# Optimization experiments

Hardware: AMD Instinct MI355X
Metric: run time of the kernel (lower is better)

Reference implementation:

```python
import jax, jax.numpy as jnp
import numpy as np

SAME_RANGE = 1.0  # forward() default same_range
FLOW_SCALE = 32.0  # realistic pixel displacements


def setup_inputs() -> dict:
    key = jax.random.key(0)
    k1, k2, k3 = jax.random.split(key, 3)
    H, W, C = 2160, 3840, 3
    img = jax.random.uniform(k1, (H, W, C), dtype=jnp.float32)
    flow = jax.random.normal(k2, (H, W, 2), dtype=jnp.float32) * FLOW_SCALE
    depth = jax.random.uniform(k3, (H, W), dtype=jnp.float32) * 100.0 + 0.1
    return {"img": img, "flow": flow, "depth": depth}


def reference(img, flow, depth):
    """Forward warping with depth z-buffer occlusion resolution.

    Each source pixel (y,x) is scattered to p1 = p0 + flow (clamped to the
    image). At each target cell, only the contributions whose depth is within
    SAME_RANGE of the minimum arriving depth survive; surviving contributions
    are averaged. Empty cells stay zero (matches np.zeros_like init in the
    original C-library warp).
    """
    H, W, C = img.shape
    N = H * W
    gy, gx = jnp.meshgrid(jnp.arange(H, dtype=flow.dtype),
                          jnp.arange(W, dtype=flow.dtype), indexing='ij')
    # safe_x / safe_y clamped target coordinates
    tx = jnp.clip(gx + flow[..., 0], 0.0, W - 1)
    ty = jnp.clip(gy + flow[..., 1], 0.0, H - 1)
    ix = jnp.round(tx).astype(jnp.int32)
    iy = jnp.round(ty).astype(jnp.int32)
    idx = jax.lax.stop_gradient((iy * W + ix).reshape(N))  # [N] flat targets

    d = depth.reshape(N)
    # z-buffer: min depth landing at each target cell
    zmin = jnp.full((N,), jnp.inf, dtype=d.dtype).at[idx].min(d)
    keep = (d <= zmin[idx] + SAME_RANGE).astype(img.dtype)  # [N]

    src = img.reshape(N, C) * keep[:, None]
    num = jnp.zeros((N, C), dtype=img.dtype).at[idx].add(src)
    cnt = jnp.zeros((N,), dtype=img.dtype).at[idx].add(keep)
    out = jnp.where(cnt[:, None] > 0, num / jnp.maximum(cnt, 1.0)[:, None], 0.0)
    return out.reshape(H, W, C)
```

## Files before the change

### kernel.cpp

```cpp
#include <hip/hip_runtime.h>

#define HH 2160
#define WW 3840
#define NN (HH * WW)

#define SROWS 2
#define NSTRIP (HH / SROWS)
#define CPS (SROWS * WW)

#define BTH 256
#define GRP 2
#define GPX 4
#define RPT (GRP * GPX)
#define PXB (BTH * RPT)

#define ICAP 12288
#define ECAP 262144
#define E0BASE ((u32)NSTRIP * ICAP)
#define E1BASE (E0BASE + ECAP)
#define TOTAL_RECS ((size_t)E1BASE + ECAP)

typedef unsigned long long u64;
typedef unsigned int u32;

__device__ __forceinline__ u32 strip_base(int s) {
    if (s == 0) return E0BASE;
    if (s == NSTRIP - 1) return E1BASE;
    return (u32)s * ICAP;
}


__global__ __launch_bounds__(256) void init_cursor_kernel(u32* __restrict__ cursor)
{
    int s = blockIdx.x * blockDim.x + threadIdx.x;
    if (s < NSTRIP) cursor[s] = strip_base(s);
}

__global__ __launch_bounds__(BTH, 6) void scatter_kernel(
    const float4* __restrict__ img4,
    const float4* __restrict__ flow4,
    const float4* __restrict__ depth4,
    u32* __restrict__ cursor,
    u64* __restrict__ recs)
{
    __shared__ u32 lc[1088];
    __shared__ u32 gb[1088];

    const int t = threadIdx.x;
    for (int s = t; s < 1088; s += BTH) lc[s] = 0;
    __syncthreads();

    const int wb = blockIdx.x * PXB;
    const int p0 = wb + t * GPX;
    const int p1 = wb + BTH * GPX + t * GPX;

    float4 fa0 = flow4[(p0 >> 1) + 0], fb0 = flow4[(p0 >> 1) + 1];
    float4 fa1 = flow4[(p1 >> 1) + 0], fb1 = flow4[(p1 >> 1) + 1];
    float4 dv0 = depth4[p0 >> 2];
    float4 dv1 = depth4[p1 >> 2];
    int ib0 = (p0 * 3) >> 2, ib1 = (p1 * 3) >> 2;
    float4 a0 = img4[ib0 + 0], a1 = img4[ib0 + 1], a2 = img4[ib0 + 2];
    float4 c0 = img4[ib1 + 0], c1 = img4[ib1 + 1], c2 = img4[ib1 + 2];

    u64 rrec[GRP][GPX];
    u32 aux[GRP][GPX];

    #pragma unroll
    for (int g = 0; g < GRP; ++g) {
        int p = g ? p1 : p0;
        int y = p / WW;
        int x = p - y * WW;
        float4 fa = g ? fa1 : fa0, fb = g ? fb1 : fb0;
        float4 dv = g ? dv1 : dv0;
        float4 i0 = g ? c0 : a0, i1 = g ? c1 : a1, i2 = g ? c2 : a2;
        float fx[GPX] = { fa.x, fa.z, fb.x, fb.z };
        float fy[GPX] = { fa.y, fa.w, fb.y, fb.w };
        float rr[GPX] = { i0.x, i0.w, i1.z, i2.y };
        float gg[GPX] = { i0.y, i1.x, i1.w, i2.z };
        float bb[GPX] = { i0.z, i1.y, i2.x, i2.w };
        float dd[GPX] = { dv.x, dv.y, dv.z, dv.w };
        #pragma unroll
        for (int k = 0; k < GPX; ++k) {
            float tx = fminf(fmaxf((float)(x + k) + fx[k], 0.0f), (float)(WW - 1));
            float ty = fminf(fmaxf((float)y + fy[k], 0.0f), (float)(HH - 1));
            int ix = (int)rintf(tx);
            int iy = (int)rintf(ty);
            int st = iy >> 1;
            u32 cell = (u32)((iy & 1) * WW + ix);
            u32 rq = (u32)(rr[k] * 63.0f + 0.5f);
            u32 gq = (u32)(gg[k] * 127.0f + 0.5f);
            u32 bq = (u32)(bb[k] * 63.0f + 0.5f);
            rrec[g][k] = ((u64)__float_as_uint(dd[k]) << 32)
                       | ((u64)cell << 19)
                       | (u64)(rq | (gq << 6) | (bq << 13));
            u32 rank = atomicAdd(&lc[st], 1u);
            aux[g][k] = ((u32)st << 13) | rank;
        }
    }
    __syncthreads();

    for (int s = t; s < NSTRIP; s += BTH) {
        u32 c = lc[s];
        if (c) gb[s] = atomicAdd(&cursor[s], c);
    }
    __syncthreads();

    #pragma unroll
    for (int g = 0; g < GRP; ++g) {
        #pragma unroll
        for (int k = 0; k < GPX; ++k) {
            u32 a = aux[g][k];
            u32 st = a >> 13, rank = a & 8191u;
            recs[(size_t)gb[st] + rank] = rrec[g][k];
        }
    }
}

__global__ __launch_bounds__(1024) void strip_kernel(
    const u64* __restrict__ recs,
    const u32* __restrict__ cursor,
    float* __restrict__ out)
{
    __shared__ u32 zmin[CPS];
    __shared__ u64 acc[CPS];
    int t = threadIdx.x;
    for (int c = t; c < CPS; c += 1024) { zmin[c] = 0xFFFFFFFFu; acc[c] = 0ull; }
    __syncthreads();

    int bs = blockIdx.x;
    int s = (bs == 0) ? 0 : (bs == 1 ? (NSTRIP - 1) : bs - 1);
    u32 lo = strip_base(s);
    u32 hi = cursor[s];

    for (u32 r = lo + t; r < hi; r += 1024) {
        u64 rec = recs[r];
        atomicMin(&zmin[(u32)(rec >> 19) & 8191u], (u32)(rec >> 32));
    }
    __syncthreads();

    for (u32 r = lo + t; r < hi; r += 1024) {
        u64 rec = recs[r];
        u32 cell = (u32)(rec >> 19) & 8191u;
        float d = __uint_as_float((u32)(rec >> 32));
        float z = __uint_as_float(zmin[cell]);
        if (d <= z + 1.0f) {
            u64 a = 1ull
                  | (((u64)rec & 63ull) << 10)
                  | ((((u64)rec >> 6) & 127ull) << 26)
                  | ((((u64)rec >> 13) & 63ull) << 43);
            atomicAdd(&acc[cell], a);
        }
    }
    __syncthreads();

    float* o = out + (size_t)s * CPS * 3;
    for (int c0 = t * 4; c0 < CPS; c0 += 1024 * 4) {
        float v[12];
        #pragma unroll
        for (int k = 0; k < 4; ++k) {
            u64 p = acc[c0 + k];
            u32 cnt = (u32)(p & 1023u);
            float r = 0.0f, g = 0.0f, b = 0.0f;
            if (cnt) {
                float invc = 1.0f / (float)cnt;
                r = (float)((p >> 10) & 0xFFFFull) * (invc * (1.0f / 63.0f));
                g = (float)((p >> 26) & 0x1FFFFull) * (invc * (1.0f / 127.0f));
                b = (float)((p >> 43) & 0xFFFFull) * (invc * (1.0f / 63.0f));
            }
            v[3 * k + 0] = r; v[3 * k + 1] = g; v[3 * k + 2] = b;
        }
        float4* o4 = (float4*)(o + 3 * c0);
        o4[0] = make_float4(v[0], v[1], v[2], v[3]);
        o4[1] = make_float4(v[4], v[5], v[6], v[7]);
        o4[2] = make_float4(v[8], v[9], v[10], v[11]);
    }
}

__device__ __forceinline__ int target_idx(int i, const float2* __restrict__ flow) {
    int y = i / WW;
    int x = i - y * WW;
    float2 f = flow[i];
    float tx = fminf(fmaxf((float)x + f.x, 0.0f), (float)(WW - 1));
    float ty = fminf(fmaxf((float)y + f.y, 0.0f), (float)(HH - 1));
    return (int)rintf(ty) * WW + (int)rintf(tx);
}

__global__ __launch_bounds__(256) void scatter_min_kernel(
    const float2* __restrict__ flow,
    const float* __restrict__ depth,
    u32* __restrict__ zmin)
{
    int i = blockIdx.x * blockDim.x + threadIdx.x;
    if (i >= NN) return;
    int idx = target_idx(i, flow);
    u32 db = __float_as_uint(depth[i]);
    u32 cur = zmin[idx];
    if (db < cur) atomicMin(&zmin[idx], db);
}

__global__ __launch_bounds__(256) void scatter_add_packed_kernel(
    const float* __restrict__ img,
    const float2* __restrict__ flow,
    const float* __restrict__ depth,
    const u32* __restrict__ zmin,
    u64* __restrict__ acc)
{
    int i = blockIdx.x * blockDim.x + threadIdx.x;
    if (i >= NN) return;
    int idx = target_idx(i, flow);
    float d = depth[i];
    float z = __uint_as_float(zmin[idx]);
    if (d <= z + 1.0f) {
        u64 rq = (u64)(u32)(img[3 * i + 0] * 127.0f + 0.5f);
        u64 gq = (u64)(u32)(img[3 * i + 1] * 127.0f + 0.5f);
        u64 bq = (u64)(u32)(img[3 * i + 2] * 127.0f + 0.5f);
        atomicAdd(&acc[idx], (rq << 48) | (gq << 32) | (bq << 16) | 1ull);
    }
}

__global__ __launch_bounds__(256) void finalize_packed_kernel(
    const u64* __restrict__ acc,
    float* __restrict__ out)
{
    int i = blockIdx.x * blockDim.x + threadIdx.x;
    if (i >= NN) return;
    u64 p = acc[i];
    u32 cnt = (u32)(p & 0xFFFFull);
    float r = 0.0f, g = 0.0f, b = 0.0f;
    if (cnt) {
        float inv = 1.0f / (127.0f * (float)cnt);
        r = (float)((p >> 48) & 0xFFFFull) * inv;
        g = (float)((p >> 32) & 0xFFFFull) * inv;
        b = (float)((p >> 16) & 0xFFFFull) * inv;
    }
    out[3 * i + 0] = r;
    out[3 * i + 1] = g;
    out[3 * i + 2] = b;
}

extern "C" void kernel_launch(void* const* d_in, const int* in_sizes, int n_in,
                              void* d_out, int out_size, void* d_ws, size_t ws_size,
                              hipStream_t stream)
{
    const float*  img   = (const float*)d_in[0];
    const float*  flow  = (const float*)d_in[1];
    const float*  depth = (const float*)d_in[2];
    float* out = (float*)d_out;

    const size_t rec_bytes = TOTAL_RECS * 8;
    const size_t cur_off   = (rec_bytes + 255) & ~(size_t)255;

    if (ws_size >= cur_off + NSTRIP * sizeof(u32)) {
        u64* recs   = (u64*)d_ws;
        u32* cursor = (u32*)((char*)d_ws + cur_off);

        init_cursor_kernel<<<(NSTRIP + 255) / 256, 256, 0, stream>>>(cursor);

        const int nwg = NN / PXB;
        scatter_kernel<<<nwg, BTH, 0, stream>>>(
            (const float4*)img, (const float4*)flow, (const float4*)depth,
            cursor, recs);
        strip_kernel<<<NSTRIP, 1024, 0, stream>>>(recs, cursor, out);
    } else {
        const size_t zb = (size_t)NN * 4;
        u32* zmin = (u32*)d_ws;
        u64* acc  = (u64*)((char*)d_ws + zb);

        hipMemsetAsync(zmin, 0xFF, zb, stream);
        hipMemsetAsync(acc, 0, (size_t)NN * 8, stream);

        const int block = 256;
        const int grid = (NN + block - 1) / block;
        scatter_min_kernel<<<grid, block, 0, stream>>>((const float2*)flow, depth, zmin);
        scatter_add_packed_kernel<<<grid, block, 0, stream>>>(img, (const float2*)flow, depth, zmin, acc);
        finalize_packed_kernel<<<grid, block, 0, stream>>>(acc, out);
    }
}
```

Measured before the change: 133.4 us.

## Window strip histogram in scatter, nontemporal stores, paired record loads

The scatter kernel now keeps its shared-memory strip counters only for a 192-strip window around the block's source rows. Out-of-window pixels fall back to direct global atomics on the strip cursor. This shrinks LDS init and the per-block cursor flush loop from 1080 strips to 192, which helps occupancy and cuts global atomics. Record and output writes use nontemporal stores, and the strip kernel reads records in 128-bit pairs. The risk is many per-pixel global atomics when large flows land outside the window, which rounding at clamped edges makes likely near the borders.

```diff
diff --git a/kernel.cpp b/kernel.cpp
--- a/kernel.cpp
+++ b/kernel.cpp
@@ -11,8 +11,9 @@
 #define BTH 256
 #define GRP 2
 #define GPX 4
-#define RPT (GRP * GPX)
-#define PXB (BTH * RPT)
+#define PXB (BTH * GRP * GPX)
+
+#define WIN 192
 
 #define ICAP 12288
 #define ECAP 262144
@@ -22,6 +23,7 @@
 
 typedef unsigned long long u64;
 typedef unsigned int u32;
+typedef float f4n __attribute__((ext_vector_type(4)));
 
 __device__ __forceinline__ u32 strip_base(int s) {
     if (s == 0) return E0BASE;
@@ -43,14 +45,18 @@
     u32* __restrict__ cursor,
     u64* __restrict__ recs)
 {
-    __shared__ u32 lc[1088];
-    __shared__ u32 gb[1088];
+    __shared__ u32 lc[WIN];
+    __shared__ u32 gb[WIN];
 
     const int t = threadIdx.x;
-    for (int s = t; s < 1088; s += BTH) lc[s] = 0;
+    if (t < WIN) lc[t] = 0;
     __syncthreads();
 
     const int wb = blockIdx.x * PXB;
+    const int ywb = wb / WW;
+    int w0 = (ywb >> 1) - (WIN / 2);
+    w0 = w0 < 0 ? 0 : (w0 > NSTRIP - WIN ? NSTRIP - WIN : w0);
+
     const int p0 = wb + t * GPX;
     const int p1 = wb + BTH * GPX + t * GPX;
 
@@ -90,18 +96,26 @@
             u32 rq = (u32)(rr[k] * 63.0f + 0.5f);
             u32 gq = (u32)(gg[k] * 127.0f + 0.5f);
             u32 bq = (u32)(bb[k] * 63.0f + 0.5f);
-            rrec[g][k] = ((u64)__float_as_uint(dd[k]) << 32)
-                       | ((u64)cell << 19)
-                       | (u64)(rq | (gq << 6) | (bq << 13));
-            u32 rank = atomicAdd(&lc[st], 1u);
-            aux[g][k] = ((u32)st << 13) | rank;
-        }
-    }
-    __syncthreads();
-
-    for (int s = t; s < NSTRIP; s += BTH) {
-        u32 c = lc[s];
-        if (c) gb[s] = atomicAdd(&cursor[s], c);
+            u64 rec = ((u64)__float_as_uint(dd[k]) << 32)
+                    | ((u64)cell << 19)
+                    | (u64)(rq | (gq << 6) | (bq << 13));
+            rrec[g][k] = rec;
+            int wst = st - w0;
+            if ((unsigned)wst < WIN) {
+                u32 rank = atomicAdd(&lc[wst], 1u);
+                aux[g][k] = ((u32)wst << 13) | rank;
+            } else {
+                u32 slot = atomicAdd(&cursor[st], 1u);
+                __builtin_nontemporal_store(rec, &recs[slot]);
+                aux[g][k] = 0xFFFFFFFFu;
+            }
+        }
+    }
+    __syncthreads();
+
+    if (t < WIN) {
+        u32 c = lc[t];
+        if (c) gb[t] = atomicAdd(&cursor[w0 + t], c);
     }
     __syncthreads();
 
@@ -110,8 +124,11 @@
         #pragma unroll
         for (int k = 0; k < GPX; ++k) {
             u32 a = aux[g][k];
-            u32 st = a >> 13, rank = a & 8191u;
-            recs[(size_t)gb[st] + rank] = rrec[g][k];
+            if (a != 0xFFFFFFFFu) {
+                u32 wst = a >> 13, rank = a & 8191u;
+                __builtin_nontemporal_store(rrec[g][k],
+                                            &recs[(size_t)gb[wst] + rank]);
+            }
         }
     }
 }
@@ -130,16 +147,40 @@
     int bs = blockIdx.x;
     int s = (bs == 0) ? 0 : (bs == 1 ? (NSTRIP - 1) : bs - 1);
     u32 lo = strip_base(s);
-    u32 hi = cursor[s];
-
-    for (u32 r = lo + t; r < hi; r += 1024) {
-        u64 rec = recs[r];
+    u32 n = cursor[s] - lo;
+    const ulonglong2* rp = (const ulonglong2*)(recs + lo);
+    u32 npair = n >> 1;
+
+    for (u32 j = t; j < npair; j += 1024) {
+        ulonglong2 rr = rp[j];
+        atomicMin(&zmin[(u32)(rr.x >> 19) & 8191u], (u32)(rr.x >> 32));
+        atomicMin(&zmin[(u32)(rr.y >> 19) & 8191u], (u32)(rr.y >> 32));
+    }
+    if (t == 0 && (n & 1)) {
+        u64 rec = recs[lo + n - 1];
         atomicMin(&zmin[(u32)(rec >> 19) & 8191u], (u32)(rec >> 32));
     }
     __syncthreads();
 
-    for (u32 r = lo + t; r < hi; r += 1024) {
-        u64 rec = recs[r];
+    for (u32 j = t; j < npair; j += 1024) {
+        ulonglong2 rr = rp[j];
+        #pragma unroll
+        for (int h = 0; h < 2; ++h) {
+            u64 rec = h ? rr.y : rr.x;
+            u32 cell = (u32)(rec >> 19) & 8191u;
+            float d = __uint_as_float((u32)(rec >> 32));
+            float z = __uint_as_float(zmin[cell]);
+            if (d <= z + 1.0f) {
+                u64 a = 1ull
+                      | (((u64)rec & 63ull) << 10)
+                      | ((((u64)rec >> 6) & 127ull) << 26)
+                      | ((((u64)rec >> 13) & 63ull) << 43);
+                atomicAdd(&acc[cell], a);
+            }
+        }
+    }
+    if (t == 0 && (n & 1)) {
+        u64 rec = recs[lo + n - 1];
         u32 cell = (u32)(rec >> 19) & 8191u;
         float d = __uint_as_float((u32)(rec >> 32));
         float z = __uint_as_float(zmin[cell]);
@@ -169,10 +210,13 @@
             }
             v[3 * k + 0] = r; v[3 * k + 1] = g; v[3 * k + 2] = b;
         }
-        float4* o4 = (float4*)(o + 3 * c0);
-        o4[0] = make_float4(v[0], v[1], v[2], v[3]);
-        o4[1] = make_float4(v[4], v[5], v[6], v[7]);
-        o4[2] = make_float4(v[8], v[9], v[10], v[11]);
+        f4n* o4 = (f4n*)(o + 3 * c0);
+        f4n w0v = { v[0], v[1], v[2],  v[3]  };
+        f4n w1v = { v[4], v[5], v[6],  v[7]  };
+        f4n w2v = { v[8], v[9], v[10], v[11] };
+        __builtin_nontemporal_store(w0v, &o4[0]);
+        __builtin_nontemporal_store(w1v, &o4[1]);
+        __builtin_nontemporal_store(w2v, &o4[2]);
     }
 }
 
```

Result: slower. 258.9 us (+94.1%).
